# Performance work log

Measured on AMD Instinct MI355X. Metric: run time of the kernel, lower is better.

The kernel has to match this reference:

```python
import jax, jax.numpy as jnp
import numpy as np

B, L, E, V = 4, 2048, 1024, 64
NT = V * (V - 1) // 2  # 2016 upper-triangular entries
LN_EPS = 1e-5


def setup_inputs() -> dict:
    key = jax.random.key(0)
    ks = jax.random.split(key, 9)
    s = lambda d: 1.0 / np.sqrt(d)
    return {
        "hx": jax.random.normal(ks[0], (B, L, E), dtype=jnp.float32),
        "W_dense": jax.random.normal(ks[1], (E, E), dtype=jnp.float32) * s(E),
        "b_dense": jnp.zeros((E,), dtype=jnp.float32),
        "ln_g": jnp.ones((E,), dtype=jnp.float32),
        "ln_b": jnp.zeros((E,), dtype=jnp.float32),
        "W_theta": jax.random.normal(ks[2], (V, E), dtype=jnp.float32) * s(E),
        "b_theta": jnp.zeros((V,), dtype=jnp.float32),
        "W_Theta": jax.random.normal(ks[3], (NT, E), dtype=jnp.float32) * s(E),
        "b_Theta": jnp.zeros((NT,), dtype=jnp.float32),
    }


def reference(hx, W_dense, b_dense, ln_g, ln_b, W_theta, b_theta, W_Theta, b_Theta):
    # dense -> exact (erf) gelu -> LayerNorm (ESM1bLayerNorm)
    h = jax.nn.gelu(hx @ W_dense.T + b_dense, approximate=False)
    mu = jnp.mean(h, axis=-1, keepdims=True)
    var = jnp.mean(jnp.square(h - mu), axis=-1, keepdims=True)
    h = (h - mu) / jnp.sqrt(var + LN_EPS) * ln_g + ln_b

    pi = jax.nn.softmax(h @ W_theta.T + b_theta, axis=-1)          # (B,L,V)
    Theta = jax.nn.softplus(h @ W_Theta.T + b_Theta)               # (B,L,NT)

    iu, ju = np.triu_indices(V, k=1)
    S = jnp.zeros((B, L, V, V), dtype=h.dtype).at[:, :, iu, ju].set(Theta)
    S = S + jnp.swapaxes(S, -2, -1)                                # symmetric, zero diag

    # diag(1/sqrt(pi)) @ S @ diag(sqrt(pi)) == S * sqrt(pi_j)/sqrt(pi_i)
    pi_sqrt = jnp.sqrt(pi)
    Q = S * (pi_sqrt[..., None, :] / pi_sqrt[..., :, None])
    Q = Q - Q.sum(axis=-1)[..., :, None] * jnp.eye(V, dtype=Q.dtype)
    return (Q, pi)
```

## Files before the change

kernel.cpp:

```cpp
#include <hip/hip_runtime.h>
#include <hip/hip_bf16.h>
#include <cstdint>
#include <cstddef>

#define MROWS 8192
#define EDIM  1024
#define VDIM  64
#define NTRI  2016
#define NTC   2176

typedef _Float16 half8  __attribute__((ext_vector_type(8)));
typedef _Float16 half4v __attribute__((ext_vector_type(4)));
typedef float    floatx4 __attribute__((ext_vector_type(4)));

typedef __attribute__((address_space(1))) void gvoid;
typedef __attribute__((address_space(3))) void svoid;

__device__ inline void gld_lds16(const _Float16* g, _Float16* l) {
    __builtin_amdgcn_global_load_lds((gvoid*)g, (svoid*)l, 16, 0, 0);
}

__device__ inline float fast_erf(float x) {
    float ax = fabsf(x);
    float t = 1.0f / (1.0f + 0.3275911f * ax);
    float p = t * (0.254829592f +
              t * (-0.284496736f +
              t * (1.421413741f +
              t * (-1.453152027f +
              t * 1.061405429f))));
    float r = 1.0f - p * __expf(-ax * ax);
    return copysignf(r, x);
}

__device__ inline float fast_softplus(float x) {
    return fmaxf(x, 0.0f) + __logf(1.0f + __expf(-fabsf(x)));
}

__global__ __launch_bounds__(256) void cast_f2h(const float* __restrict__ in,
                                                _Float16* __restrict__ out,
                                                int n_valid, int n_total) {
    int idx = (blockIdx.x * 256 + threadIdx.x) * 4;
    if (idx >= n_total) return;
    half4v o;
    if (idx < n_valid) {
        float4 v = *(const float4*)(in + idx);
        o[0] = (_Float16)v.x; o[1] = (_Float16)v.y;
        o[2] = (_Float16)v.z; o[3] = (_Float16)v.w;
    } else {
        o[0] = (_Float16)0.f; o[1] = (_Float16)0.f;
        o[2] = (_Float16)0.f; o[3] = (_Float16)0.f;
    }
    *(half4v*)(out + idx) = o;
}

template <int MODE>
__global__ __launch_bounds__(256) void gemm_bt(const _Float16* __restrict__ A,
                                               const _Float16* __restrict__ Bt,
                                               const float* __restrict__ bias,
                                               const float* __restrict__ bias2,
                                               _Float16* __restrict__ C, int N) {
    __shared__ __align__(16) _Float16 As[128 * 64];
    __shared__ __align__(16) _Float16 Bs[128 * 64];

    const int tid  = threadIdx.x;
    const int ng   = N >> 7;
    const int xcd  = blockIdx.x & 7;
    const int slot = blockIdx.x >> 3;
    const int mg   = slot / ng;
    const int nn   = slot - mg * ng;
    const int m0   = (xcd + mg * 8) * 128;
    const int n0   = nn * 128;

    const int w    = tid >> 6;
    const int lane = tid & 63;
    const int wr   = w >> 1;
    const int wc   = w & 1;
    const int lrow  = lane & 15;
    const int lquad = lane >> 4;

    floatx4 acc[4][4] = {};

    const int r0 = tid >> 3;
    const int c0 = tid & 7;
    const int g  = (c0 ^ (r0 & 7)) * 8;
    const _Float16* Ag[4];
    const _Float16* Bg[4];
#pragma unroll
    for (int call = 0; call < 4; ++call) {
        Ag[call] = A  + (size_t)(m0 + call * 32 + r0) * EDIM + g;
        Bg[call] = Bt + (size_t)(n0 + call * 32 + r0) * EDIM + g;
    }
    _Float16* AsD = &As[tid * 8];
    _Float16* BsD = &Bs[tid * 8];

    const int swr = lrow & 7;
    const _Float16* ardA = &As[(wr * 64 + lrow) * 64];
    const _Float16* brdB = &Bs[(wc * 64 + lrow) * 64];

    for (int k0 = 0; k0 < EDIM; k0 += 64) {
#pragma unroll
        for (int call = 0; call < 4; ++call) {
            gld_lds16(Ag[call] + k0, AsD + call * 2048);
            gld_lds16(Bg[call] + k0, BsD + call * 2048);
        }
        __syncthreads();

#pragma unroll
        for (int kstep = 0; kstep < 2; ++kstep) {
            const int soff = ((kstep * 4 + lquad) ^ swr) * 8;
            half8 af[4], bf[4];
#pragma unroll
            for (int t = 0; t < 4; ++t) {
                af[t] = *(const half8*)(ardA + t * 16 * 64 + soff);
                bf[t] = *(const half8*)(brdB + t * 16 * 64 + soff);
            }
#pragma unroll
            for (int i = 0; i < 4; ++i)
#pragma unroll
                for (int j = 0; j < 4; ++j)
                    acc[i][j] = __builtin_amdgcn_mfma_f32_16x16x32_f16(
                        af[i], bf[j], acc[i][j], 0, 0, 0);
        }
        __syncthreads();
    }

    const int cm = m0 + wr * 64 + lquad * 4;
    const int cn = n0 + wc * 64 + lrow;
#pragma unroll
    for (int j = 0; j < 4; ++j) {
        const int gn = cn + j * 16;
        float bv;
        if (MODE == 0) {
            bv = bias[gn];
        } else {
            if (gn < NTRI)             bv = bias[gn];
            else if (gn < NTRI + VDIM) bv = bias2[gn - NTRI];
            else                       bv = 0.0f;
        }
#pragma unroll
        for (int i = 0; i < 4; ++i) {
#pragma unroll
            for (int r = 0; r < 4; ++r) {
                float x = acc[i][j][r] + bv;
                float y;
                if (MODE == 0) {
                    y = 0.5f * x * (1.0f + fast_erf(x * 0.70710678118654752f));
                } else {
                    if (gn < NTRI) {
                        y = fast_softplus(x);
                    } else if (gn < NTRI + VDIM) {
                        y = x;
                    } else {
                        y = 0.0f;
                    }
                }
                C[(size_t)(cm + i * 16 + r) * N + gn] = (_Float16)y;
            }
        }
    }
}

__global__ __launch_bounds__(256) void ln_kernel(const _Float16* __restrict__ G,
                                                 const float* __restrict__ gw,
                                                 const float* __restrict__ bw,
                                                 _Float16* __restrict__ Hh) {
    const int row = blockIdx.x, tid = threadIdx.x;
    half4v v = ((const half4v*)(G + (size_t)row * EDIM))[tid];
    float x0 = (float)v[0], x1 = (float)v[1], x2 = (float)v[2], x3 = (float)v[3];
    float s  = x0 + x1 + x2 + x3;
    float ss = x0 * x0 + x1 * x1 + x2 * x2 + x3 * x3;
#pragma unroll
    for (int off = 32; off; off >>= 1) {
        s  += __shfl_down(s, off);
        ss += __shfl_down(ss, off);
    }
    __shared__ float red[8];
    const int w = tid >> 6, lane = tid & 63;
    if (lane == 0) { red[w] = s; red[4 + w] = ss; }
    __syncthreads();
    const float st  = red[0] + red[1] + red[2] + red[3];
    const float sst = red[4] + red[5] + red[6] + red[7];
    const float mu  = st * (1.0f / EDIM);
    const float rs  = 1.0f / sqrtf(sst * (1.0f / EDIM) - mu * mu + 1e-5f);
    float4 gg = ((const float4*)gw)[tid];
    float4 bb = ((const float4*)bw)[tid];
    half4v h4;
    h4[0] = (_Float16)((x0 - mu) * rs * gg.x + bb.x);
    h4[1] = (_Float16)((x1 - mu) * rs * gg.y + bb.y);
    h4[2] = (_Float16)((x2 - mu) * rs * gg.z + bb.z);
    h4[3] = (_Float16)((x3 - mu) * rs * gg.w + bb.w);
    ((half4v*)(Hh + (size_t)row * EDIM))[tid] = h4;
}

__global__ __launch_bounds__(256) void q_kernel(const _Float16* __restrict__ Theta,
                                                float* __restrict__ pi_out,
                                                float* __restrict__ Q) {
    const int row = blockIdx.x;
    const int tid = threadIdx.x;
    __shared__ float Th[NTRI];
    __shared__ float spv[VDIM];
    const _Float16* trow = Theta + (size_t)row * NTC;
    if (tid < 252) {
        half8 h = *(const half8*)(trow + tid * 8);
#pragma unroll
        for (int u = 0; u < 8; ++u) Th[tid * 8 + u] = (float)h[u];
    }
    if (tid >= 192) {
        const int lane = tid & 63;
        float lg = (float)trow[NTRI + lane];
        float m = lg;
#pragma unroll
        for (int off = 32; off; off >>= 1) m = fmaxf(m, __shfl_xor(m, off));
        float e = __expf(lg - m);
        float ssum = e;
#pragma unroll
        for (int off = 32; off; off >>= 1) ssum += __shfl_xor(ssum, off);
        float p = e / ssum;
        pi_out[(size_t)row * VDIM + lane] = p;
        spv[lane] = sqrtf(p);
    }
    __syncthreads();

    const int i = tid >> 2;
    const int q = tid & 3;
    const float rpi = 1.0f / spv[i];
    float vals[16];
    float psum = 0.f;
#pragma unroll
    for (int c = 0; c < 16; ++c) {
        const int j = q * 16 + c;
        float out = 0.f;
        if (j != i) {
            const int a = (i < j) ? i : j;
            const int b = (i < j) ? j : i;
            const int t = a * (127 - a) / 2 + (b - a - 1);
            out = Th[t] * spv[j] * rpi;
            psum += out;
        }
        vals[c] = out;
    }
    psum += __shfl_xor(psum, 1);
    psum += __shfl_xor(psum, 2);
    if ((i >> 4) == q) vals[i & 15] = -psum;

    float* qrow = Q + ((size_t)row * VDIM + i) * VDIM + q * 16;
    float4* dst = (float4*)qrow;
    dst[0] = make_float4(vals[0], vals[1], vals[2], vals[3]);
    dst[1] = make_float4(vals[4], vals[5], vals[6], vals[7]);
    dst[2] = make_float4(vals[8], vals[9], vals[10], vals[11]);
    dst[3] = make_float4(vals[12], vals[13], vals[14], vals[15]);
}

extern "C" void kernel_launch(void* const* d_in, const int* in_sizes, int n_in,
                              void* d_out, int out_size, void* d_ws, size_t ws_size,
                              hipStream_t stream) {
    const float* hx      = (const float*)d_in[0];
    const float* W_dense = (const float*)d_in[1];
    const float* b_dense = (const float*)d_in[2];
    const float* ln_g    = (const float*)d_in[3];
    const float* ln_b    = (const float*)d_in[4];
    const float* W_theta = (const float*)d_in[5];
    const float* b_theta = (const float*)d_in[6];
    const float* W_Theta = (const float*)d_in[7];
    const float* b_Theta = (const float*)d_in[8];

    uint8_t* ws = (uint8_t*)d_ws;
    _Float16* A_h  = (_Float16*)ws;
    _Float16* Wd_h = (_Float16*)(ws + (size_t)16 * 1048576);
    _Float16* Wc_h = (_Float16*)(ws + (size_t)18 * 1048576);
    _Float16* G_h  = (_Float16*)(ws + (size_t)23 * 1048576);
    _Float16* Th_h = (_Float16*)(ws + (size_t)23 * 1048576);

    float* Q_out  = (float*)d_out;
    float* pi_out = (float*)d_out + (size_t)MROWS * VDIM * VDIM;

    cast_f2h<<<(MROWS * EDIM / 4) / 256, 256, 0, stream>>>(hx, A_h, MROWS * EDIM, MROWS * EDIM);
    cast_f2h<<<(EDIM * EDIM / 4) / 256, 256, 0, stream>>>(W_dense, Wd_h, EDIM * EDIM, EDIM * EDIM);
    cast_f2h<<<(NTRI * EDIM / 4) / 256, 256, 0, stream>>>(W_Theta, Wc_h, NTRI * EDIM, NTRI * EDIM);
    cast_f2h<<<((NTC - NTRI) * EDIM / 4) / 256, 256, 0, stream>>>(
        W_theta, Wc_h + (size_t)NTRI * EDIM, VDIM * EDIM, (NTC - NTRI) * EDIM);

    gemm_bt<0><<<(EDIM / 128) * (MROWS / 128), 256, 0, stream>>>(
        A_h, Wd_h, b_dense, nullptr, G_h, EDIM);

    ln_kernel<<<MROWS, 256, 0, stream>>>(G_h, ln_g, ln_b, A_h);

    gemm_bt<1><<<(NTC / 128) * (MROWS / 128), 256, 0, stream>>>(
        A_h, Wc_h, b_Theta, b_theta, Th_h, NTC);

    q_kernel<<<MROWS, 256, 0, stream>>>(Th_h, pi_out, Q_out);
}
```

Measured before the change: 320.4 us.

## Replace GEMM with 256-row tiled, 4-stage LDS-pipelined 8-wave kernel

Replaces the single-buffered 128x128 GEMM with a 512-thread kernel that uses 256-row tiles and a 4-deep ring of LDS buffers. Global-to-LDS loads for tile t+3 are issued while MFMAs run on tile t, with explicit vmcnt waits, barriers, and setprio around the MFMA bursts. The second GEMM is split into a 2048-column launch with wider tiles plus a small tail launch for the remaining 128 columns. This aims to hide memory latency and increase reuse per loaded tile, at the cost of more LDS, more registers, and hand-tuned wait counts that are fragile.

```diff
diff --git a/kernel.cpp b/kernel.cpp
--- a/kernel.cpp
+++ b/kernel.cpp
@@ -19,6 +19,10 @@
 __device__ inline void gld_lds16(const _Float16* g, _Float16* l) {
     __builtin_amdgcn_global_load_lds((gvoid*)g, (svoid*)l, 16, 0, 0);
 }
+
+#define BAR() do { asm volatile("" ::: "memory"); \
+                   __builtin_amdgcn_s_barrier();  \
+                   asm volatile("" ::: "memory"); } while (0)
 
 __device__ inline float fast_erf(float x) {
     float ax = fabsf(x);
@@ -53,82 +57,123 @@
     *(half4v*)(out + idx) = o;
 }
 
-template <int MODE>
-__global__ __launch_bounds__(256) void gemm_bt(const _Float16* __restrict__ A,
-                                               const _Float16* __restrict__ Bt,
-                                               const float* __restrict__ bias,
-                                               const float* __restrict__ bias2,
-                                               _Float16* __restrict__ C, int N) {
-    __shared__ __align__(16) _Float16 As[128 * 64];
-    __shared__ __align__(16) _Float16 Bs[128 * 64];
+template <int MODE, int NF>
+__global__ __launch_bounds__(512, 2) void gemm25(const _Float16* __restrict__ A,
+                                                 const _Float16* __restrict__ Bt,
+                                                 const float* __restrict__ bias,
+                                                 const float* __restrict__ bias2,
+                                                 _Float16* __restrict__ C,
+                                                 int ldC, int col0, int ntg) {
+    constexpr int BN = NF * 64;
+    constexpr int WN = NF * 16;
+    constexpr int BHALF = 8192 + BN * 32;
+    constexpr int NT = EDIM / 32;
+    __shared__ __align__(16) _Float16 S[4][BHALF];
 
     const int tid  = threadIdx.x;
-    const int ng   = N >> 7;
     const int xcd  = blockIdx.x & 7;
     const int slot = blockIdx.x >> 3;
-    const int mg   = slot / ng;
-    const int nn   = slot - mg * ng;
-    const int m0   = (xcd + mg * 8) * 128;
-    const int n0   = nn * 128;
-
-    const int w    = tid >> 6;
-    const int lane = tid & 63;
-    const int wr   = w >> 1;
-    const int wc   = w & 1;
-    const int lrow  = lane & 15;
-    const int lquad = lane >> 4;
-
-    floatx4 acc[4][4] = {};
-
-    const int r0 = tid >> 3;
-    const int c0 = tid & 7;
-    const int g  = (c0 ^ (r0 & 7)) * 8;
-    const _Float16* Ag[4];
-    const _Float16* Bg[4];
-#pragma unroll
-    for (int call = 0; call < 4; ++call) {
-        Ag[call] = A  + (size_t)(m0 + call * 32 + r0) * EDIM + g;
-        Bg[call] = Bt + (size_t)(n0 + call * 32 + r0) * EDIM + g;
-    }
-    _Float16* AsD = &As[tid * 8];
-    _Float16* BsD = &Bs[tid * 8];
-
-    const int swr = lrow & 7;
-    const _Float16* ardA = &As[(wr * 64 + lrow) * 64];
-    const _Float16* brdB = &Bs[(wc * 64 + lrow) * 64];
-
-    for (int k0 = 0; k0 < EDIM; k0 += 64) {
-#pragma unroll
-        for (int call = 0; call < 4; ++call) {
-            gld_lds16(Ag[call] + k0, AsD + call * 2048);
-            gld_lds16(Bg[call] + k0, BsD + call * 2048);
-        }
-        __syncthreads();
-
-#pragma unroll
-        for (int kstep = 0; kstep < 2; ++kstep) {
-            const int soff = ((kstep * 4 + lquad) ^ swr) * 8;
-            half8 af[4], bf[4];
-#pragma unroll
-            for (int t = 0; t < 4; ++t) {
-                af[t] = *(const half8*)(ardA + t * 16 * 64 + soff);
-                bf[t] = *(const half8*)(brdB + t * 16 * 64 + soff);
-            }
-#pragma unroll
-            for (int i = 0; i < 4; ++i)
-#pragma unroll
-                for (int j = 0; j < 4; ++j)
-                    acc[i][j] = __builtin_amdgcn_mfma_f32_16x16x32_f16(
-                        af[i], bf[j], acc[i][j], 0, 0, 0);
-        }
-        __syncthreads();
-    }
-
-    const int cm = m0 + wr * 64 + lquad * 4;
-    const int cn = n0 + wc * 64 + lrow;
-#pragma unroll
-    for (int j = 0; j < 4; ++j) {
-        const int gn = cn + j * 16;
+    const int nn   = slot % ntg;
+    const int mg   = slot / ntg;
+    const int m0   = (xcd + mg * 8) * 256;
+    const int n0   = nn * BN;
+
+    const int w = tid >> 6, lane = tid & 63;
+    const int wr = w >> 2;
+    const int wc = w & 3;
+    const int lrow = lane & 15, lquad = lane >> 4;
+
+    floatx4 acc[8][NF] = {};
+
+    const int R  = tid >> 2;
+    const int c0 = tid & 3;
+    const int gk = (c0 ^ ((R >> 1) & 3)) * 8;
+    const _Float16* Ag0 = A  + (size_t)(m0 + R) * EDIM + gk;
+    const _Float16* Ag1 = Ag0 + (size_t)128 * EDIM;
+    const _Float16* Bg0 = Bt + (size_t)(col0 + n0 + R) * EDIM + gk;
+    const _Float16* Bg1 = Bg0 + (size_t)128 * EDIM;
+
+    const int xr   = (lrow >> 1) & 3;
+    const int koff = (lquad ^ xr) * 8;
+    const int aoff = (wr * 128 + lrow) * 32 + koff;
+    const int boff = 8192 + (wc * WN + lrow) * 32 + koff;
+
+#pragma unroll
+    for (int t = 0; t < 3; ++t) {
+        _Float16* d = &S[t][tid * 8];
+        gld_lds16(Ag0 + t * 32, d);
+        gld_lds16(Ag1 + t * 32, d + 4096);
+        gld_lds16(Bg0 + t * 32, d + 8192);
+        if constexpr (NF == 4) gld_lds16(Bg1 + t * 32, d + 12288);
+    }
+    if constexpr (NF == 4) asm volatile("s_waitcnt vmcnt(8)" ::: "memory");
+    else                   asm volatile("s_waitcnt vmcnt(6)" ::: "memory");
+    BAR();
+
+#pragma unroll 1
+    for (int t = 0; t < NT; ++t) {
+        const int buf = t & 3;
+        const _Float16* Sb = S[buf];
+        const bool doStage = (t + 3 < NT);
+        const int sb = (t + 3) & 3;
+        const int sk = (t + 3) * 32;
+
+        half8 bf[NF], af[4];
+#pragma unroll
+        for (int j = 0; j < NF; ++j) bf[j] = *(const half8*)(Sb + boff + j * 512);
+#pragma unroll
+        for (int i = 0; i < 4; ++i)  af[i] = *(const half8*)(Sb + aoff + i * 512);
+        if (doStage) {
+            _Float16* d = &S[sb][tid * 8];
+            gld_lds16(Ag0 + sk, d);
+            gld_lds16(Ag1 + sk, d + 4096);
+        }
+        BAR();
+        __builtin_amdgcn_s_setprio(1);
+#pragma unroll
+        for (int i = 0; i < 4; ++i)
+#pragma unroll
+            for (int j = 0; j < NF; ++j)
+                acc[i][j] = __builtin_amdgcn_mfma_f32_16x16x32_f16(
+                    af[i], bf[j], acc[i][j], 0, 0, 0);
+        __builtin_amdgcn_s_setprio(0);
+        BAR();
+
+#pragma unroll
+        for (int i = 0; i < 4; ++i)
+            af[i] = *(const half8*)(Sb + aoff + 2048 + i * 512);
+        if (doStage) {
+            _Float16* d = &S[sb][tid * 8];
+            gld_lds16(Bg0 + sk, d + 8192);
+            if constexpr (NF == 4) gld_lds16(Bg1 + sk, d + 12288);
+        }
+        BAR();
+        __builtin_amdgcn_s_setprio(1);
+#pragma unroll
+        for (int i = 0; i < 4; ++i)
+#pragma unroll
+            for (int j = 0; j < NF; ++j)
+                acc[4 + i][j] = __builtin_amdgcn_mfma_f32_16x16x32_f16(
+                    af[i], bf[j], acc[4 + i][j], 0, 0, 0);
+        __builtin_amdgcn_s_setprio(0);
+
+        if (t < NT - 3) {
+            if constexpr (NF == 4) asm volatile("s_waitcnt vmcnt(8)" ::: "memory");
+            else                   asm volatile("s_waitcnt vmcnt(6)" ::: "memory");
+        } else if (t == NT - 3) {
+            if constexpr (NF == 4) asm volatile("s_waitcnt vmcnt(4)" ::: "memory");
+            else                   asm volatile("s_waitcnt vmcnt(3)" ::: "memory");
+        } else if (t == NT - 2) {
+            asm volatile("s_waitcnt vmcnt(0)" ::: "memory");
+        }
+        BAR();
+    }
+
+    const int cmb = m0 + wr * 128 + lquad * 4;
+    const int cnb = col0 + n0 + wc * WN + lrow;
+#pragma unroll
+    for (int j = 0; j < NF; ++j) {
+        const int gn = cnb + j * 16;
         float bv;
         if (MODE == 0) {
             bv = bias[gn];
@@ -138,7 +183,7 @@
             else                       bv = 0.0f;
         }
 #pragma unroll
-        for (int i = 0; i < 4; ++i) {
+        for (int i = 0; i < 8; ++i) {
 #pragma unroll
             for (int r = 0; r < 4; ++r) {
                 float x = acc[i][j][r] + bv;
@@ -146,15 +191,11 @@
                 if (MODE == 0) {
                     y = 0.5f * x * (1.0f + fast_erf(x * 0.70710678118654752f));
                 } else {
-                    if (gn < NTRI) {
-                        y = fast_softplus(x);
-                    } else if (gn < NTRI + VDIM) {
-                        y = x;
-                    } else {
-                        y = 0.0f;
-                    }
+                    if (gn < NTRI)             y = fast_softplus(x);
+                    else if (gn < NTRI + VDIM) y = x;
+                    else                       y = 0.0f;
                 }
-                C[(size_t)(cm + i * 16 + r) * N + gn] = (_Float16)y;
+                C[(size_t)(cmb + i * 16 + r) * ldC + gn] = (_Float16)y;
             }
         }
     }
@@ -280,13 +321,12 @@
     cast_f2h<<<((NTC - NTRI) * EDIM / 4) / 256, 256, 0, stream>>>(
         W_theta, Wc_h + (size_t)NTRI * EDIM, VDIM * EDIM, (NTC - NTRI) * EDIM);
 
-    gemm_bt<0><<<(EDIM / 128) * (MROWS / 128), 256, 0, stream>>>(
-        A_h, Wd_h, b_dense, nullptr, G_h, EDIM);
+    gemm25<0, 2><<<256, 512, 0, stream>>>(A_h, Wd_h, b_dense, nullptr, G_h, EDIM, 0, 8);
 
     ln_kernel<<<MROWS, 256, 0, stream>>>(G_h, ln_g, ln_b, A_h);
 
-    gemm_bt<1><<<(NTC / 128) * (MROWS / 128), 256, 0, stream>>>(
-        A_h, Wc_h, b_Theta, b_theta, Th_h, NTC);
+    gemm25<1, 4><<<256, 512, 0, stream>>>(A_h, Wc_h, b_Theta, b_theta, Th_h, NTC, 0, 8);
+    gemm25<1, 2><<<32, 512, 0, stream>>>(A_h, Wc_h, b_Theta, b_theta, Th_h, NTC, 2048, 1);
 
     q_kernel<<<MROWS, 256, 0, stream>>>(Th_h, pi_out, Q_out);
 }
```

New measurement: 325.0 us. About the same (+1.4%).

## Triple-buffer GEMM K-loop with async LDS loads and merge cast kernels

Applied to the files above, without the earlier changes.

Rewrites both GEMMs to use a three-stage LDS ring with K tiles of 32. Global-to-LDS loads run two tiles ahead, governed by explicit vmcnt waits and a single barrier per step instead of two syncthreads. MFMA sections are wrapped in setprio, and launch bounds now ask for three blocks per CU. The four fp32-to-fp16 cast launches are merged into one kernel to cut launch overhead. The cost is hand-managed wait counts and more LDS per block, which may limit occupancy.

```diff
diff --git a/kernel.cpp b/kernel.cpp
--- a/kernel.cpp
+++ b/kernel.cpp
@@ -36,92 +36,119 @@
     return fmaxf(x, 0.0f) + __logf(1.0f + __expf(-fabsf(x)));
 }
 
-__global__ __launch_bounds__(256) void cast_f2h(const float* __restrict__ in,
-                                                _Float16* __restrict__ out,
-                                                int n_valid, int n_total) {
-    int idx = (blockIdx.x * 256 + threadIdx.x) * 4;
-    if (idx >= n_total) return;
+__global__ __launch_bounds__(256) void cast_all(const float* __restrict__ hx,
+                                                const float* __restrict__ Wd,
+                                                const float* __restrict__ WT,
+                                                const float* __restrict__ wt,
+                                                _Float16* __restrict__ A_h,
+                                                _Float16* __restrict__ Wd_h,
+                                                _Float16* __restrict__ Wc_h) {
+    const int b = blockIdx.x;
+    float4 v;
+    _Float16* dst;
+    int idx;
+    if (b < 8192) {
+        idx = (b * 256 + threadIdx.x) * 4;
+        v = *(const float4*)(hx + idx);
+        dst = A_h;
+    } else if (b < 9216) {
+        idx = ((b - 8192) * 256 + threadIdx.x) * 4;
+        v = *(const float4*)(Wd + idx);
+        dst = Wd_h;
+    } else {
+        idx = ((b - 9216) * 256 + threadIdx.x) * 4;
+        if (idx < NTRI * EDIM)                  v = *(const float4*)(WT + idx);
+        else if (idx < (NTRI + VDIM) * EDIM)    v = *(const float4*)(wt + (idx - NTRI * EDIM));
+        else                                    v = make_float4(0.f, 0.f, 0.f, 0.f);
+        dst = Wc_h;
+    }
     half4v o;
-    if (idx < n_valid) {
-        float4 v = *(const float4*)(in + idx);
-        o[0] = (_Float16)v.x; o[1] = (_Float16)v.y;
-        o[2] = (_Float16)v.z; o[3] = (_Float16)v.w;
-    } else {
-        o[0] = (_Float16)0.f; o[1] = (_Float16)0.f;
-        o[2] = (_Float16)0.f; o[3] = (_Float16)0.f;
-    }
-    *(half4v*)(out + idx) = o;
+    o[0] = (_Float16)v.x; o[1] = (_Float16)v.y;
+    o[2] = (_Float16)v.z; o[3] = (_Float16)v.w;
+    *(half4v*)(dst + idx) = o;
 }
 
 template <int MODE>
-__global__ __launch_bounds__(256) void gemm_bt(const _Float16* __restrict__ A,
-                                               const _Float16* __restrict__ Bt,
-                                               const float* __restrict__ bias,
-                                               const float* __restrict__ bias2,
-                                               _Float16* __restrict__ C, int N) {
-    __shared__ __align__(16) _Float16 As[128 * 64];
-    __shared__ __align__(16) _Float16 Bs[128 * 64];
+__global__ __launch_bounds__(256, 3) void gemm128(const _Float16* __restrict__ A,
+                                                  const _Float16* __restrict__ Bt,
+                                                  const float* __restrict__ bias,
+                                                  const float* __restrict__ bias2,
+                                                  _Float16* __restrict__ C,
+                                                  int ldC, int ntg) {
+    constexpr int NT = EDIM / 32;
+    __shared__ __align__(16) _Float16 S[3][8192];
 
     const int tid  = threadIdx.x;
-    const int ng   = N >> 7;
     const int xcd  = blockIdx.x & 7;
     const int slot = blockIdx.x >> 3;
-    const int mg   = slot / ng;
-    const int nn   = slot - mg * ng;
+    const int mg   = slot / ntg;
+    const int nn   = slot - mg * ntg;
     const int m0   = (xcd + mg * 8) * 128;
     const int n0   = nn * 128;
 
-    const int w    = tid >> 6;
-    const int lane = tid & 63;
-    const int wr   = w >> 1;
-    const int wc   = w & 1;
-    const int lrow  = lane & 15;
-    const int lquad = lane >> 4;
+    const int w = tid >> 6, lane = tid & 63;
+    const int wr = w >> 1, wc = w & 1;
+    const int lrow = lane & 15, lquad = lane >> 4;
 
     floatx4 acc[4][4] = {};
 
-    const int r0 = tid >> 3;
-    const int c0 = tid & 7;
-    const int g  = (c0 ^ (r0 & 7)) * 8;
-    const _Float16* Ag[4];
-    const _Float16* Bg[4];
-#pragma unroll
-    for (int call = 0; call < 4; ++call) {
-        Ag[call] = A  + (size_t)(m0 + call * 32 + r0) * EDIM + g;
-        Bg[call] = Bt + (size_t)(n0 + call * 32 + r0) * EDIM + g;
-    }
-    _Float16* AsD = &As[tid * 8];
-    _Float16* BsD = &Bs[tid * 8];
-
-    const int swr = lrow & 7;
-    const _Float16* ardA = &As[(wr * 64 + lrow) * 64];
-    const _Float16* brdB = &Bs[(wc * 64 + lrow) * 64];
-
-    for (int k0 = 0; k0 < EDIM; k0 += 64) {
-#pragma unroll
-        for (int call = 0; call < 4; ++call) {
-            gld_lds16(Ag[call] + k0, AsD + call * 2048);
-            gld_lds16(Bg[call] + k0, BsD + call * 2048);
+    const int r0 = tid >> 2;
+    const int c0 = tid & 3;
+    const int gk = (c0 ^ ((r0 >> 1) & 3)) * 8;
+    const _Float16* Ag0 = A  + (size_t)(m0 + r0) * EDIM + gk;
+    const _Float16* Ag1 = Ag0 + (size_t)64 * EDIM;
+    const _Float16* Bg0 = Bt + (size_t)(n0 + r0) * EDIM + gk;
+    const _Float16* Bg1 = Bg0 + (size_t)64 * EDIM;
+
+    const int xr   = (lrow >> 1) & 3;
+    const int koff = (lquad ^ xr) * 8;
+    const int aoff = (wr * 64 + lrow) * 32 + koff;
+    const int boff = 4096 + (wc * 64 + lrow) * 32 + koff;
+
+    auto stage = [&](int buf, int kt) {
+        _Float16* d = &S[buf][tid * 8];
+        const int ko = kt * 32;
+        gld_lds16(Ag0 + ko, d);
+        gld_lds16(Ag1 + ko, d + 2048);
+        gld_lds16(Bg0 + ko, d + 4096);
+        gld_lds16(Bg1 + ko, d + 6144);
+    };
+
+    stage(0, 0);
+    stage(1, 1);
+    asm volatile("s_waitcnt vmcnt(4)" ::: "memory");
+    __builtin_amdgcn_s_barrier();
+
+    int buf = 0, sbuf = 2;
+#pragma unroll 1
+    for (int t = 0; t < NT; ++t) {
+        const _Float16* Sb = S[buf];
+        if (t + 2 < NT) stage(sbuf, t + 2);
+
+        half8 af[4], bf[4];
+#pragma unroll
+        for (int i = 0; i < 4; ++i) af[i] = *(const half8*)(Sb + aoff + i * 512);
+#pragma unroll
+        for (int j = 0; j < 4; ++j) bf[j] = *(const half8*)(Sb + boff + j * 512);
+
+        __builtin_amdgcn_s_setprio(1);
+#pragma unroll
+        for (int i = 0; i < 4; ++i)
+#pragma unroll
+            for (int j = 0; j < 4; ++j)
+                acc[i][j] = __builtin_amdgcn_mfma_f32_16x16x32_f16(
+                    af[i], bf[j], acc[i][j], 0, 0, 0);
+        __builtin_amdgcn_s_setprio(0);
+
+        if (t < NT - 2)       asm volatile("s_waitcnt vmcnt(4)" ::: "memory");
+        else if (t == NT - 2) asm volatile("s_waitcnt vmcnt(0)" ::: "memory");
+        if (t < NT - 1) {
+            asm volatile("" ::: "memory");
+            __builtin_amdgcn_s_barrier();
+            asm volatile("" ::: "memory");
         }
-        __syncthreads();
-
-#pragma unroll
-        for (int kstep = 0; kstep < 2; ++kstep) {
-            const int soff = ((kstep * 4 + lquad) ^ swr) * 8;
-            half8 af[4], bf[4];
-#pragma unroll
-            for (int t = 0; t < 4; ++t) {
-                af[t] = *(const half8*)(ardA + t * 16 * 64 + soff);
-                bf[t] = *(const half8*)(brdB + t * 16 * 64 + soff);
-            }
-#pragma unroll
-            for (int i = 0; i < 4; ++i)
-#pragma unroll
-                for (int j = 0; j < 4; ++j)
-                    acc[i][j] = __builtin_amdgcn_mfma_f32_16x16x32_f16(
-                        af[i], bf[j], acc[i][j], 0, 0, 0);
-        }
-        __syncthreads();
+        buf  = (buf  == 2) ? 0 : buf + 1;
+        sbuf = (sbuf == 2) ? 0 : sbuf + 1;
     }
 
     const int cm = m0 + wr * 64 + lquad * 4;
@@ -146,15 +173,11 @@
                 if (MODE == 0) {
                     y = 0.5f * x * (1.0f + fast_erf(x * 0.70710678118654752f));
                 } else {
-                    if (gn < NTRI) {
-                        y = fast_softplus(x);
-                    } else if (gn < NTRI + VDIM) {
-                        y = x;
-                    } else {
-                        y = 0.0f;
-                    }
+                    if (gn < NTRI)             y = fast_softplus(x);
+                    else if (gn < NTRI + VDIM) y = x;
+                    else                       y = 0.0f;
                 }
-                C[(size_t)(cm + i * 16 + r) * N + gn] = (_Float16)y;
+                C[(size_t)(cm + i * 16 + r) * ldC + gn] = (_Float16)y;
             }
         }
     }
@@ -274,19 +297,14 @@
     float* Q_out  = (float*)d_out;
     float* pi_out = (float*)d_out + (size_t)MROWS * VDIM * VDIM;
 
-    cast_f2h<<<(MROWS * EDIM / 4) / 256, 256, 0, stream>>>(hx, A_h, MROWS * EDIM, MROWS * EDIM);
-    cast_f2h<<<(EDIM * EDIM / 4) / 256, 256, 0, stream>>>(W_dense, Wd_h, EDIM * EDIM, EDIM * EDIM);
-    cast_f2h<<<(NTRI * EDIM / 4) / 256, 256, 0, stream>>>(W_Theta, Wc_h, NTRI * EDIM, NTRI * EDIM);
-    cast_f2h<<<((NTC - NTRI) * EDIM / 4) / 256, 256, 0, stream>>>(
-        W_theta, Wc_h + (size_t)NTRI * EDIM, VDIM * EDIM, (NTC - NTRI) * EDIM);
-
-    gemm_bt<0><<<(EDIM / 128) * (MROWS / 128), 256, 0, stream>>>(
-        A_h, Wd_h, b_dense, nullptr, G_h, EDIM);
+    cast_all<<<11392, 256, 0, stream>>>(hx, W_dense, W_Theta, W_theta,
+                                        A_h, Wd_h, Wc_h);
+
+    gemm128<0><<<512, 256, 0, stream>>>(A_h, Wd_h, b_dense, nullptr, G_h, EDIM, 8);
 
     ln_kernel<<<MROWS, 256, 0, stream>>>(G_h, ln_g, ln_b, A_h);
 
-    gemm_bt<1><<<(NTC / 128) * (MROWS / 128), 256, 0, stream>>>(
-        A_h, Wc_h, b_Theta, b_theta, Th_h, NTC);
+    gemm128<1><<<1088, 256, 0, stream>>>(A_h, Wc_h, b_Theta, b_theta, Th_h, NTC, 17);
 
     q_kernel<<<MROWS, 256, 0, stream>>>(Th_h, pi_out, Q_out);
 }
```

New measurement: 307.7 us. 1.04x faster.
